# Kernel tuning notes

Measured on AMD Instinct MI355X. Metric: run time of the kernel, lower is better.

The kernel has to match this reference:

```python
import jax, jax.numpy as jnp
import numpy as np

EPS = 1e-6

def _rms(x, scale):
    # flax nn.RMSNorm: x / sqrt(mean(x^2)+eps) * scale, no mean subtraction
    return x * scale * jax.lax.rsqrt(jnp.mean(x * x, axis=-1, keepdims=True) + EPS)


def _forward(x, mem_k, mem_v, norm1_scale, norm2_scale,
             Wq, bq, Wk, bk, Wv, bv, Wz, bz,
             Wgz, bgz, Wgh, bgh,
             Wg1, bg1, Wg2, bg2, Wgc1, bgc1, Wgc2, bgc2,
             Awq, abq, Awk, abk, Awv, abv, Awo, abo,
             Wf1, bf1, Wf2, bf2):
    B, S, D = x.shape
    M = mem_k.shape[1]
    H = 8
    hd = D // H

    x_norm = _rms(x, norm1_scale)
    q = x_norm @ Wq + bq
    k = x_norm @ Wk + bk
    v = x_norm @ Wv + bv
    z = x_norm @ Wz + bz

    # input-dependent decay gamma in (1e-6, 1-1e-6)
    gamma_base = jax.nn.sigmoid(jax.nn.gelu(z @ Wg1 + bg1) @ Wg2 + bg2)
    gamma_mod = jax.nn.sigmoid(jax.nn.gelu(k @ Wgc1 + bgc1) @ Wgc2 + bgc2)
    gamma = jnp.clip(gamma_base * gamma_mod, 1e-6, 1.0 - 1e-6)

    # gated leaky recurrence over sequence: h depends on W_g_h(h_prev) -> strict scan
    def step(h_prev, zt_gt):
        z_t, g_t = zt_gt  # [B, D] each
        gate = jax.nn.sigmoid(z_t @ Wgz + bgz + h_prev @ Wgh + bgh)
        h_tilde = (1.0 - gate) * h_prev + gate * z_t
        h_t = h_tilde + g_t * h_prev
        return h_t, h_t

    h0 = jnp.zeros((B, D), dtype=x.dtype)
    z_T = jnp.swapaxes(z, 0, 1)          # [S, B, D]
    gamma_T = jnp.swapaxes(gamma, 0, 1)  # [S, B, D]
    _, h_seq_T = jax.lax.scan(step, h0, (z_T, gamma_T))
    h_seq = jnp.swapaxes(h_seq_T, 0, 1)  # [B, S, D]

    # MultiMemoryAttention: q from q_input, K/V from memory state banks [B, M, D]
    qh = (q @ Awq + abq).reshape(B, S, H, hd)
    kh = (mem_k @ Awk + abk).reshape(B, M, H, hd)
    vh = (mem_v @ Awv + abv).reshape(B, M, H, hd)
    scores = jnp.einsum('bshd,bmhd->bhsm', qh, kh) / jnp.sqrt(jnp.asarray(hd, x.dtype))
    probs = jax.nn.softmax(scores, axis=-1)
    mem_out = jnp.einsum('bhsm,bmhd->bshd', probs, vh).reshape(B, S, D) @ Awo + abo

    combined = h_seq + mem_out + v * 0.1
    x_res = x + combined  # dropout deterministic (training=False)

    x_norm2 = _rms(x_res, norm2_scale)
    ffn = jax.nn.gelu(x_norm2 @ Wf1 + bf1) @ Wf2 + bf2
    return x_res + ffn


def setup_inputs() -> dict:
    key = jax.random.key(0)
    B, S, D, H, F, M = 4, 4096, 1024, 8, 4096, 512
    Dq = D // 4
    ks = jax.random.split(key, 24)
    def w(i, shape):
        return jax.random.normal(ks[i], shape, dtype=jnp.float32) * 0.02
    d = {
        'x': jax.random.normal(ks[0], (B, S, D), dtype=jnp.float32),
        'mem_k': jax.random.normal(ks[1], (B, M, D), dtype=jnp.float32),
        'mem_v': jax.random.normal(ks[2], (B, M, D), dtype=jnp.float32),
        'norm1_scale': jnp.ones((D,), jnp.float32),
        'norm2_scale': jnp.ones((D,), jnp.float32),
        'Wq': w(3, (D, D)), 'bq': jnp.zeros((D,), jnp.float32),
        'Wk': w(4, (D, D)), 'bk': jnp.zeros((D,), jnp.float32),
        'Wv': w(5, (D, D)), 'bv': jnp.zeros((D,), jnp.float32),
        'Wz': w(6, (D, D)), 'bz': jnp.zeros((D,), jnp.float32),
        'Wgz': w(7, (D, D)), 'bgz': jnp.zeros((D,), jnp.float32),
        'Wgh': w(8, (D, D)), 'bgh': jnp.zeros((D,), jnp.float32),
        'Wg1': w(9, (D, Dq)), 'bg1': jnp.zeros((Dq,), jnp.float32),
        'Wg2': w(10, (Dq, D)), 'bg2': jnp.zeros((D,), jnp.float32),
        'Wgc1': w(11, (D, Dq)), 'bgc1': jnp.zeros((Dq,), jnp.float32),
        'Wgc2': w(12, (Dq, D)), 'bgc2': jnp.zeros((D,), jnp.float32),
        'Awq': w(13, (D, D)), 'abq': jnp.zeros((D,), jnp.float32),
        'Awk': w(14, (D, D)), 'abk': jnp.zeros((D,), jnp.float32),
        'Awv': w(15, (D, D)), 'abv': jnp.zeros((D,), jnp.float32),
        'Awo': w(16, (D, D)), 'abo': jnp.zeros((D,), jnp.float32),
        'Wf1': w(17, (D, F)), 'bf1': jnp.zeros((F,), jnp.float32),
        'Wf2': w(18, (F, D)), 'bf2': jnp.zeros((D,), jnp.float32),
    }
    return d


def reference(x, mem_k, mem_v, norm1_scale, norm2_scale,
              Wq, bq, Wk, bk, Wv, bv, Wz, bz,
              Wgz, bgz, Wgh, bgh,
              Wg1, bg1, Wg2, bg2, Wgc1, bgc1, Wgc2, bgc2,
              Awq, abq, Awk, abk, Awv, abv, Awo, abo,
              Wf1, bf1, Wf2, bf2):
    return _forward(x, mem_k, mem_v, norm1_scale, norm2_scale,
                    Wq, bq, Wk, bk, Wv, bv, Wz, bz,
                    Wgz, bgz, Wgh, bgh,
                    Wg1, bg1, Wg2, bg2, Wgc1, bgc1, Wgc2, bgc2,
                    Awq, abq, Awk, abk, Awv, abv, Awo, abo,
                    Wf1, bf1, Wf2, bf2)
```

## Files before the change

kernel.cpp:

```cpp
#include <hip/hip_runtime.h>
#include <stdint.h>

typedef short s16x8 __attribute__((ext_vector_type(8)));
typedef float f32x4 __attribute__((ext_vector_type(4)));

#define DEV static __device__ __forceinline__

DEV float bf2f(ushort u){ union{uint i;float f;}v; v.i=((uint)u)<<16; return v.f; }
DEV ushort f2bf(float f){ union{float f;uint i;}v; v.f=f; return (ushort)((v.i + 0x7FFFu + ((v.i>>16)&1u))>>16); }
DEV float fsigmoid(float x){ return 1.f/(1.f+__expf(-x)); }
DEV float fgelu(float x){
  float u = 0.7978845608028654f*(x + 0.044715f*x*x*x);
  float e = __expf(2.f*u);
  float th = 1.f - 2.f/(e+1.f);
  return 0.5f*x*(1.f+th);
}
DEV f32x4 mfma16(s16x8 a, s16x8 b, f32x4 c){
  return __builtin_amdgcn_mfma_f32_16x16x32_bf16(a,b,c,0,0,0);
}

__global__ __launch_bounds__(256) void transpose_cvt(const float* __restrict__ src,
                                                     ushort* __restrict__ dst, int K, int N){
  __shared__ float tile[64][65];
  int tk = blockIdx.y*64, tn = blockIdx.x*64;
  int t = threadIdx.x;
  int c4 = (t & 15)*4, r0 = t >> 4;
  #pragma unroll
  for (int p=0;p<4;++p){
    int r = r0 + p*16;
    float4 v = *(const float4*)(src + (size_t)(tk+r)*N + tn + c4);
    tile[r][c4+0]=v.x; tile[r][c4+1]=v.y; tile[r][c4+2]=v.z; tile[r][c4+3]=v.w;
  }
  __syncthreads();
  #pragma unroll
  for (int p=0;p<4;++p){
    int n = r0 + p*16;
    ushort4 o = make_ushort4(f2bf(tile[c4+0][n]), f2bf(tile[c4+1][n]),
                             f2bf(tile[c4+2][n]), f2bf(tile[c4+3][n]));
    *(ushort4*)(dst + (size_t)(tn+n)*K + tk + c4) = o;
  }
}

__global__ __launch_bounds__(256) void cvt_bf16(const float* __restrict__ s,
                                                ushort* __restrict__ d, int n){
  int i = (blockIdx.x*256 + threadIdx.x)*4;
  if (i < n){
    float4 v = *(const float4*)(s + i);
    ushort4 o = make_ushort4(f2bf(v.x), f2bf(v.y), f2bf(v.z), f2bf(v.w));
    *(ushort4*)(d + i) = o;
  }
}

__global__ __launch_bounds__(256) void bias_sum_k(const float* __restrict__ a,
                                                  const float* __restrict__ b,
                                                  float* __restrict__ o){
  int i = blockIdx.x*256 + threadIdx.x;
  if (i < 1024) o[i] = a[i] + b[i];
}

__global__ __launch_bounds__(256) void fuse_bias(const float* __restrict__ b_in,
                                                 const float* __restrict__ W,
                                                 const float* __restrict__ b_out,
                                                 float* __restrict__ o, int K, int N){
  int n = blockIdx.x*256 + threadIdx.x;
  if (n < N){
    float s = b_out[n];
    for (int k=0;k<K;++k) s += b_in[k]*W[(size_t)k*N + n];
    o[n] = s;
  }
}

__global__ __launch_bounds__(256) void rms_kernel(const float* __restrict__ x,
                                                  const float* __restrict__ scale,
                                                  ushort* __restrict__ out){
  int row = blockIdx.x, t = threadIdx.x;
  const float* xr = x + (size_t)row*1024;
  float4 v = *(const float4*)(xr + t*4);
  float ss = v.x*v.x + v.y*v.y + v.z*v.z + v.w*v.w;
  #pragma unroll
  for (int o=1;o<64;o<<=1) ss += __shfl_xor(ss, o);
  __shared__ float wsum[4];
  if ((t & 63)==0) wsum[t>>6] = ss;
  __syncthreads();
  float tot = wsum[0]+wsum[1]+wsum[2]+wsum[3];
  float rstd = rsqrtf(tot*(1.f/1024.f) + 1e-6f);
  float4 sc = *(const float4*)(scale + t*4);
  ushort4 o4 = make_ushort4(f2bf(v.x*sc.x*rstd), f2bf(v.y*sc.y*rstd),
                            f2bf(v.z*sc.z*rstd), f2bf(v.w*sc.w*rstd));
  *(ushort4*)(out + (size_t)row*1024 + t*4) = o4;
}

template<int EPI>
__global__ __launch_bounds__(256,2) void gemm_bf16(
    const ushort* __restrict__ A, const ushort* __restrict__ Bt,
    const float* __restrict__ bias, void* __restrict__ Cout,
    const void* __restrict__ aux0, const void* __restrict__ aux1,
    int M, int N, int K)
{
  __shared__ ushort Al[128*32];
  __shared__ ushort Bl[128*32];
  const int t = threadIdx.x, ln = t & 63;
  const int m0 = blockIdx.y*128, n0 = blockIdx.x*128;
  const int wv = t >> 6, wr = wv >> 1, wc = wv & 1;
  const int lr = ln & 15, lk = ln >> 4;
  f32x4 acc[4][4] = {};
  for (int kk = 0; kk < K; kk += 32) {
    #pragma unroll
    for (int cc = 0; cc < 2; ++cc) {
      int e = cc*256 + t;
      int r = e >> 2, sg = e & 3;
      s16x8 va = *(const s16x8*)(A  + (size_t)(m0+r)*K + kk + sg*8);
      s16x8 vb = *(const s16x8*)(Bt + (size_t)(n0+r)*K + kk + sg*8);
      *(s16x8*)&Al[e*8] = va;
      *(s16x8*)&Bl[e*8] = vb;
    }
    __syncthreads();
    s16x8 af[4], bfr[4];
    #pragma unroll
    for (int m=0;m<4;++m) af[m]  = *(const s16x8*)&Al[(wr*64 + m*16 + lr)*32 + lk*8];
    #pragma unroll
    for (int n=0;n<4;++n) bfr[n] = *(const s16x8*)&Bl[(wc*64 + n*16 + lr)*32 + lk*8];
    #pragma unroll
    for (int m=0;m<4;++m)
      #pragma unroll
      for (int n=0;n<4;++n)
        acc[m][n] = mfma16(af[m], bfr[n], acc[m][n]);
    __syncthreads();
  }
  #pragma unroll
  for (int m=0;m<4;++m){
    #pragma unroll
    for (int n=0;n<4;++n){
      #pragma unroll
      for (int j=0;j<4;++j){
        int row = m0 + wr*64 + m*16 + lk*4 + j;
        int col = n0 + wc*64 + n*16 + lr;
        float v = acc[m][n][j] + (bias ? bias[col] : 0.f);
        size_t idx = (size_t)row*N + col;
        if constexpr (EPI==0){ ((ushort*)Cout)[idx] = f2bf(v); }
        else if constexpr (EPI==1){ ((ushort*)Cout)[idx] = f2bf(fgelu(v)); }
        else if constexpr (EPI==2){ ((ushort*)Cout)[idx] = f2bf(fsigmoid(v)); }
        else if constexpr (EPI==3){
          float g = fsigmoid(v) * bf2f(((const ushort*)aux0)[idx]);
          g = fminf(fmaxf(g, 1e-6f), 1.f-1e-6f);
          ((ushort*)Cout)[idx] = f2bf(g);
        }
        else if constexpr (EPI==4){
          float o = v + ((const float*)aux0)[idx] + 0.1f*bf2f(((const ushort*)aux1)[idx]);
          ((float*)Cout)[idx] = o;
        }
        else if constexpr (EPI==5){ ((float*)Cout)[idx] += v; }
        else if constexpr (EPI==6){
          int bb = row >> 9, mm = row & 511, hh = col >> 7, dd = col & 127;
          ((ushort*)Cout)[ (((size_t)(bb*8 + hh)*128 + dd) << 9) + mm ] = f2bf(v);
        }
        else if constexpr (EPI==7){
          ((ushort*)Cout)[(size_t)col*M + row] = f2bf(v);
        }
      }
    }
  }
}

__global__ __launch_bounds__(256,1) void attn_kernel(
  const ushort* __restrict__ qh, const ushort* __restrict__ kh,
  const ushort* __restrict__ vhT, ushort* __restrict__ att)
{
  __shared__ ushort P[4*16*512];
  const int t = threadIdx.x, ln = t & 63, wv = t >> 6;
  const int lr = ln & 15, lk = ln >> 4;
  const int b = blockIdx.z, h = blockIdx.y, s0 = blockIdx.x*64;

  const ushort* qrow = qh + (size_t)(b*4096 + s0 + wv*16 + lr)*1024 + h*128 + lk*8;
  s16x8 qf[4];
  #pragma unroll
  for (int kt=0;kt<4;++kt) qf[kt] = *(const s16x8*)(qrow + kt*32);
  __syncthreads();

  f32x4 zero4 = {0.f,0.f,0.f,0.f};
  f32x4 sacc[32];
  #pragma unroll
  for (int i=0;i<32;++i) sacc[i] = zero4;

  const ushort* kbase = kh + (size_t)(b*512)*1024 + h*128 + lk*8;
  #pragma unroll
  for (int mt=0;mt<32;++mt){
    const ushort* krow = kbase + (size_t)(mt*16 + lr)*1024;
    #pragma unroll
    for (int kt=0;kt<4;++kt){
      s16x8 kf = *(const s16x8*)(krow + kt*32);
      sacc[mt] = mfma16(qf[kt], kf, sacc[mt]);
    }
  }
  const float scale = 0.08838834764831845f;
  float inv[4];
  #pragma unroll
  for (int j=0;j<4;++j){
    float m = -3.4e38f;
    #pragma unroll
    for (int mt=0;mt<32;++mt) m = fmaxf(m, sacc[mt][j]);
    m = fmaxf(m, __shfl_xor(m,1)); m = fmaxf(m, __shfl_xor(m,2));
    m = fmaxf(m, __shfl_xor(m,4)); m = fmaxf(m, __shfl_xor(m,8));
    float s = 0.f;
    #pragma unroll
    for (int mt=0;mt<32;++mt){
      float p = __expf((sacc[mt][j]-m)*scale);
      sacc[mt][j] = p; s += p;
    }
    s += __shfl_xor(s,1); s += __shfl_xor(s,2);
    s += __shfl_xor(s,4); s += __shfl_xor(s,8);
    inv[j] = 1.f/s;
  }
  char* pb = (char*)P + wv*16384;
  #pragma unroll
  for (int j=0;j<4;++j){
    int row = lk*4 + j;
    uint xr = (uint)((row & 7) << 4);
    #pragma unroll
    for (int mt=0;mt<32;++mt){
      int col = mt*16 + lr;
      *(ushort*)(pb + row*1024 + (((uint)(col*2)) ^ xr)) = f2bf(sacc[mt][j]);
    }
  }
  f32x4 oacc[8];
  #pragma unroll
  for (int i=0;i<8;++i) oacc[i] = zero4;
  const ushort* vb = vhT + (size_t)(b*8 + h)*128*512;
  const char* prow = (char*)P + wv*16384 + lr*1024;
  uint xrr = (uint)((lr & 7) << 4);
  #pragma unroll
  for (int km=0;km<16;++km){
    s16x8 pf = *(const s16x8*)(prow + (((uint)((km*32 + lk*8)*2)) ^ xrr));
    #pragma unroll
    for (int dt=0;dt<8;++dt){
      s16x8 vf = *(const s16x8*)(vb + (size_t)(dt*16 + lr)*512 + km*32 + lk*8);
      oacc[dt] = mfma16(pf, vf, oacc[dt]);
    }
  }
  ushort* ob = att + (size_t)(b*4096 + s0 + wv*16)*1024 + h*128;
  #pragma unroll
  for (int dt=0;dt<8;++dt){
    #pragma unroll
    for (int j=0;j<4;++j){
      int row = lk*4 + j, col = dt*16 + lr;
      ob[(size_t)row*1024 + col] = f2bf(oacc[dt][j]*inv[j]);
    }
  }
}

#define SCAN_NB 64
__global__ __launch_bounds__(256,1) void scan_kernel(
  const float* __restrict__ Wgh,
  const ushort* __restrict__ u_bf, const ushort* __restrict__ z_bf,
  const ushort* __restrict__ g_bf, float* __restrict__ xres,
  unsigned long long* __restrict__ h_buf)
{
  __shared__ ushort WL[16*1032];
  __shared__ ushort HL[5*1032];
  __shared__ float  red[4][16][4];
  const int t = threadIdx.x, blk = blockIdx.x;
  const int ln = t & 63, wv = t >> 6;

  {
    const int c = t & 15, i0 = (t >> 4) * 64;
    for (int j = 0; j < 64; ++j) {
      int i = i0 + j;
      WL[c*1032 + i] = f2bf(Wgh[(size_t)i*1024 + blk*16 + c]);
    }
  }
  for (int e = t; e < 1032; e += 256) HL[4*1032 + e] = 0;

  float hmine = 0.f;
  const int c_ep = t & 15, b_ep = t >> 4;
  float uu=0.f, zz=0.f, gg=0.f, xv=0.f;
  if (t < 64) {
    size_t i0 = ((size_t)(b_ep*4096))*1024 + blk*16 + c_ep;
    uu = bf2f(u_bf[i0]); zz = bf2f(z_bf[i0]); gg = bf2f(g_bf[i0]); xv = xres[i0];
  }
  __syncthreads();

  const int arow = ln & 15, akc = ln >> 4;
  const ushort* Abase = &HL[(arow < 4 ? arow : 4)*1032 + akc*8];
  const ushort* Bbase = &WL[(ln & 15)*1032 + akc*8];
  const int hb_t = t >> 6, hk0 = (t & 63)*16;

  for (int step = 0; step < 4096; ++step) {
    {
      const unsigned long long* hs = h_buf + (size_t)(step & 1)*2048 + t*8;
      unsigned long long v[8];
      #pragma unroll
      for (int j = 0; j < 8; ++j)
        v[j] = __hip_atomic_load(hs + j, __ATOMIC_RELAXED, __HIP_MEMORY_SCOPE_AGENT);
      while (true) {
        uint bad = 0;
        #pragma unroll
        for (int j = 0; j < 8; ++j)
          if ((uint)(v[j] >> 32) != (uint)step) bad |= (1u << j);
        if (!bad) break;
        #pragma unroll
        for (int j = 0; j < 8; ++j)
          if (bad & (1u << j))
            v[j] = __hip_atomic_load(hs + j, __ATOMIC_RELAXED, __HIP_MEMORY_SCOPE_AGENT);
      }
      uint* dst = (uint*)&HL[hb_t*1032 + hk0];
      *(uint4*)(dst + 0) = make_uint4((uint)v[0], (uint)v[1], (uint)v[2], (uint)v[3]);
      *(uint4*)(dst + 4) = make_uint4((uint)v[4], (uint)v[5], (uint)v[6], (uint)v[7]);
    }
    __syncthreads();
    f32x4 acc = {0.f,0.f,0.f,0.f};
    #pragma unroll
    for (int m = 0; m < 8; ++m) {
      int koff = wv*256 + m*32;
      s16x8 a = *(const s16x8*)(Abase + koff);
      s16x8 b = *(const s16x8*)(Bbase + koff);
      acc = mfma16(a, b, acc);
    }
    if (ln < 16) *(f32x4*)&red[wv][ln][0] = acc;
    __syncthreads();
    if (t < 64) {
      float y = red[0][c_ep][b_ep] + red[1][c_ep][b_ep]
              + red[2][c_ep][b_ep] + red[3][c_ep][b_ep];
      float gate = fsigmoid(y + uu);
      float hn = hmine + gate*(zz - hmine) + gg*hmine;
      hmine = hn;
      int colg = blk*16 + c_ep;
      float hup = __shfl_down(hn, 1);
      if ((t & 1) == 0) {
        unsigned long long pk = ((unsigned long long)(uint)(step+1) << 32)
                              | ((uint)f2bf(hup) << 16) | (uint)f2bf(hn);
        __hip_atomic_store(h_buf + (size_t)((step+1)&1)*2048 + b_ep*512 + (colg>>1), pk,
                           __ATOMIC_RELAXED, __HIP_MEMORY_SCOPE_AGENT);
      }
      size_t idx = ((size_t)(b_ep*4096 + step))*1024 + colg;
      xres[idx] = xv + hn;
      int sn = (step+1 < 4096) ? step+1 : 4095;
      size_t idxn = ((size_t)(b_ep*4096 + sn))*1024 + colg;
      uu = bf2f(u_bf[idxn]); zz = bf2f(z_bf[idxn]); gg = bf2f(g_bf[idxn]);
      xv = xres[idxn];
    }
  }
}

extern "C" void kernel_launch(void* const* d_in, const int* in_sizes, int n_in,
                              void* d_out, int out_size, void* d_ws, size_t ws_size,
                              hipStream_t stream)
{
  const float* x    = (const float*)d_in[0];
  const float* memk = (const float*)d_in[1];
  const float* memv = (const float*)d_in[2];
  const float* n1s  = (const float*)d_in[3];
  const float* n2s  = (const float*)d_in[4];
  const float* Wq = (const float*)d_in[5];   const float* bq = (const float*)d_in[6];
  const float* Wk = (const float*)d_in[7];   const float* bk = (const float*)d_in[8];
  const float* Wv = (const float*)d_in[9];   const float* bv = (const float*)d_in[10];
  const float* Wz = (const float*)d_in[11];  const float* bz = (const float*)d_in[12];
  const float* Wgz = (const float*)d_in[13]; const float* bgz = (const float*)d_in[14];
  const float* Wgh = (const float*)d_in[15]; const float* bgh = (const float*)d_in[16];
  const float* Wg1 = (const float*)d_in[17]; const float* bg1 = (const float*)d_in[18];
  const float* Wg2 = (const float*)d_in[19]; const float* bg2 = (const float*)d_in[20];
  const float* Wgc1 = (const float*)d_in[21]; const float* bgc1 = (const float*)d_in[22];
  const float* Wgc2 = (const float*)d_in[23]; const float* bgc2 = (const float*)d_in[24];
  const float* Awq = (const float*)d_in[25]; const float* abq = (const float*)d_in[26];
  const float* Awk = (const float*)d_in[27]; const float* abk = (const float*)d_in[28];
  const float* Awv = (const float*)d_in[29]; const float* abv = (const float*)d_in[30];
  const float* Awo = (const float*)d_in[31]; const float* abo = (const float*)d_in[32];
  const float* Wf1 = (const float*)d_in[33]; const float* bf1 = (const float*)d_in[34];
  const float* Wf2 = (const float*)d_in[35]; const float* bf2 = (const float*)d_in[36];
  (void)in_sizes; (void)n_in; (void)out_size; (void)ws_size;

  char* ws = (char*)d_ws;
  constexpr size_t MB = 1ull<<20;
  ushort* WvT     = (ushort*)(ws + 0*MB);
  ushort* WzT     = (ushort*)(ws + 2*MB);
  ushort* WgzT    = (ushort*)(ws + 4*MB);
  ushort* WqAwqT  = (ushort*)(ws + 6*MB);
  ushort* AwkT    = (ushort*)(ws + 8*MB);
  ushort* AwvT    = (ushort*)(ws + 10*MB);
  ushort* AwoT    = (ushort*)(ws + 12*MB);
  ushort* Wf1T    = (ushort*)(ws + 14*MB);
  ushort* Wf2Tc   = (ushort*)(ws + 22*MB);
  ushort* Wg1T    = (ushort*)(ws + 30*MB);
  ushort* Wg2T    = (ushort*)(ws + 30*MB + 512*1024);
  ushort* Wgc2T   = (ushort*)(ws + 31*MB);
  ushort* WkWgc1T = (ushort*)(ws + 31*MB + 512*1024);
  float* bsum = (float*)(ws + 32*MB);
  float* bqh  = (float*)(ws + 32*MB + 4096);
  float* bkg  = (float*)(ws + 32*MB + 8192);
  char*  scanB = ws + 32*MB + 65536;
  ushort* Abuf = (ushort*)(ws + 33*MB);
  ushort* Bbuf = (ushort*)(ws + 65*MB);
  ushort* Cbuf = (ushort*)(ws + 97*MB);
  ushort* Dbuf = (ushort*)(ws + 129*MB);
  ushort* Ebuf = (ushort*)(ws + 161*MB);
  char* db = (char*)d_out;
  ushort* t1B   = (ushort*)(db + 0);
  ushort* memkB = (ushort*)(db + 8*MB);
  ushort* memvB = (ushort*)(db + 12*MB);
  ushort* khB   = (ushort*)(db + 16*MB);
  ushort* vhTB  = (ushort*)(db + 20*MB);
  ushort* gbB   = (ushort*)(db + 24*MB);
  ushort* WtmpB = (ushort*)(db + 56*MB);
  ushort* BtTB  = (ushort*)(db + 58*MB);

  const int M1 = 16384;
  dim3 b256(256);
  auto T = [&](const float* s, ushort* d, int K, int N){
    transpose_cvt<<<dim3(N/64, K/64), b256, 0, stream>>>(s, d, K, N);
  };
  #define G(EPI, Ap, Bp, bi, Cp, a0, a1, Mv, Nv, Kv) \
    gemm_bf16<EPI><<<dim3((Nv)/128,(Mv)/128), b256, 0, stream>>>( \
      (const ushort*)(Ap), (const ushort*)(Bp), bi, (void*)(Cp), a0, a1, Mv, Nv, Kv)

  cvt_bf16<<<1024, b256, 0, stream>>>(Wq, WtmpB, 1048576);
  T(Awq, BtTB, 1024, 1024);
  G(7, WtmpB, BtTB, nullptr, WqAwqT, nullptr, nullptr, 1024, 1024, 1024);
  fuse_bias<<<4, b256, 0, stream>>>(bq, Awq, abq, bqh, 1024, 1024);
  cvt_bf16<<<1024, b256, 0, stream>>>(Wk, WtmpB, 1048576);
  T(Wgc1, BtTB, 1024, 256);
  G(7, WtmpB, BtTB, nullptr, WkWgc1T, nullptr, nullptr, 1024, 256, 1024);
  fuse_bias<<<1, b256, 0, stream>>>(bk, Wgc1, bgc1, bkg, 1024, 256);
  T(Wv,WvT,1024,1024); T(Wz,WzT,1024,1024); T(Wgz,WgzT,1024,1024);
  T(Wg1,Wg1T,1024,256); T(Wg2,Wg2T,256,1024); T(Wgc2,Wgc2T,256,1024);
  T(Awk,AwkT,1024,1024); T(Awv,AwvT,1024,1024); T(Awo,AwoT,1024,1024);
  T(Wf1,Wf1T,1024,4096);
  for (int cch = 0; cch < 4; ++cch)
    T(Wf2 + (size_t)cch*1048576, Wf2Tc + (size_t)cch*1048576, 1024, 1024);
  bias_sum_k<<<4, b256, 0, stream>>>(bgz, bgh, bsum);
  cvt_bf16<<<2048, b256, 0, stream>>>(memk, memkB, 2097152);
  cvt_bf16<<<2048, b256, 0, stream>>>(memv, memvB, 2097152);

  rms_kernel<<<M1, b256, 0, stream>>>(x, n1s, Abuf);
  G(0, Abuf, WzT, bz, Bbuf, nullptr, nullptr, M1, 1024, 1024);
  G(0, Abuf, WvT, bv, Cbuf, nullptr, nullptr, M1, 1024, 1024);
  G(0, Abuf, WqAwqT, bqh, Dbuf, nullptr, nullptr, M1, 1024, 1024);
  G(0, Bbuf, WgzT, bsum, Ebuf, nullptr, nullptr, M1, 1024, 1024);
  G(1, Bbuf, Wg1T, bg1, t1B, nullptr, nullptr, M1, 256, 1024);
  G(2, t1B, Wg2T, bg2, gbB, nullptr, nullptr, M1, 1024, 256);
  G(1, Abuf, WkWgc1T, bkg, t1B, nullptr, nullptr, M1, 256, 1024);
  G(3, t1B, Wgc2T, bgc2, Abuf, gbB, nullptr, M1, 1024, 256);
  G(0, memkB, AwkT, abk, khB, nullptr, nullptr, 2048, 1024, 1024);
  G(6, memvB, AwvT, abv, vhTB, nullptr, nullptr, 2048, 1024, 1024);
  attn_kernel<<<dim3(64,8,4), b256, 0, stream>>>(Dbuf, khB, vhTB, Dbuf);
  G(4, Dbuf, AwoT, abo, d_out, (const void*)x, (const void*)Cbuf, M1, 1024, 1024);
  hipMemsetAsync(scanB, 0, 32768, stream);
  scan_kernel<<<SCAN_NB, b256, 0, stream>>>(Wgh, Ebuf, Bbuf, Abuf, (float*)d_out,
                                            (unsigned long long*)scanB);
  rms_kernel<<<M1, b256, 0, stream>>>((const float*)d_out, n2s, Cbuf);
  for (int cch = 0; cch < 4; ++cch) {
    G(1, Cbuf, Wf1T + (size_t)cch*1048576, bf1 + cch*1024, Dbuf, nullptr, nullptr, M1, 1024, 1024);
    G(5, Dbuf, Wf2Tc + (size_t)cch*1048576, (cch==0 ? bf2 : nullptr), d_out, nullptr, nullptr, M1, 1024, 1024);
  }
  #undef G
}
```

Baseline: 13.31 ms.

## Process scan batches separately to pipeline cross-block h exchange per batch

The scan kernel now splits each time step into four per-batch sub-steps. Each sub-step waits only on that batch's slice of the shared h buffer and prefetches the next batch's slice while the current matmul runs. This is meant to let blocks run on partial data instead of waiting for all four batches, hiding the cross-block flag latency. In exchange there are four times as many __syncthreads and MFMA passes per step, with only one useful row per pass.

```diff
diff --git a/kernel.cpp b/kernel.cpp
--- a/kernel.cpp
+++ b/kernel.cpp
@@ -256,87 +256,90 @@
   unsigned long long* __restrict__ h_buf)
 {
   __shared__ ushort WL[16*1032];
-  __shared__ ushort HL[5*1032];
-  __shared__ float  red[4][16][4];
+  __shared__ ushort HL[2*1032];
+  __shared__ float  red[4][16];
   const int t = threadIdx.x, blk = blockIdx.x;
   const int ln = t & 63, wv = t >> 6;
 
   {
-    const int c = t & 15, i0 = (t >> 4) * 64;
+    const int c = t & 15, i0q = (t >> 4) * 64;
     for (int j = 0; j < 64; ++j) {
-      int i = i0 + j;
+      int i = i0q + j;
       WL[c*1032 + i] = f2bf(Wgh[(size_t)i*1024 + blk*16 + c]);
     }
   }
-  for (int e = t; e < 1032; e += 256) HL[4*1032 + e] = 0;
-
-  float hmine = 0.f;
-  const int c_ep = t & 15, b_ep = t >> 4;
-  float uu=0.f, zz=0.f, gg=0.f, xv=0.f;
-  if (t < 64) {
-    size_t i0 = ((size_t)(b_ep*4096))*1024 + blk*16 + c_ep;
-    uu = bf2f(u_bf[i0]); zz = bf2f(z_bf[i0]); gg = bf2f(g_bf[i0]); xv = xres[i0];
-  }
+  for (int e = t; e < 1032; e += 256) HL[1032 + e] = 0;
+
+  float hst[4] = {0.f,0.f,0.f,0.f};
+  float uu[4], zz[4], gg[4], xv[4];
+  if (t < 16) {
+    #pragma unroll
+    for (int b=0;b<4;++b){
+      size_t i0 = ((size_t)(b*4096))*1024 + blk*16 + t;
+      uu[b]=bf2f(u_bf[i0]); zz[b]=bf2f(z_bf[i0]);
+      gg[b]=bf2f(g_bf[i0]); xv[b]=xres[i0];
+    }
+  }
+  const int arow = ln & 15, akc = ln >> 4;
+  const ushort* Ab = (arow == 0) ? &HL[akc*8] : &HL[1032 + akc*8];
+  const ushort* Bb = &WL[arow*1032 + akc*8];
+
+  unsigned long long p0, p1;
+  p0 = __hip_atomic_load(h_buf + t*2 + 0, __ATOMIC_RELAXED, __HIP_MEMORY_SCOPE_AGENT);
+  p1 = __hip_atomic_load(h_buf + t*2 + 1, __ATOMIC_RELAXED, __HIP_MEMORY_SCOPE_AGENT);
   __syncthreads();
 
-  const int arow = ln & 15, akc = ln >> 4;
-  const ushort* Abase = &HL[(arow < 4 ? arow : 4)*1032 + akc*8];
-  const ushort* Bbase = &WL[(ln & 15)*1032 + akc*8];
-  const int hb_t = t >> 6, hk0 = (t & 63)*16;
-
-  for (int step = 0; step < 4096; ++step) {
-    {
-      const unsigned long long* hs = h_buf + (size_t)(step & 1)*2048 + t*8;
-      unsigned long long v[8];
+  for (int s = 0; s < 4096; ++s) {
+    #pragma unroll
+    for (int b = 0; b < 4; ++b) {
+      const unsigned long long* hs =
+        h_buf + (size_t)((s & 1)*2048 + b*512) + t*2;
+      while (((uint)(p0 >> 32) != (uint)s) | ((uint)(p1 >> 32) != (uint)s)) {
+        if ((uint)(p0 >> 32) != (uint)s)
+          p0 = __hip_atomic_load(hs + 0, __ATOMIC_RELAXED, __HIP_MEMORY_SCOPE_AGENT);
+        if ((uint)(p1 >> 32) != (uint)s)
+          p1 = __hip_atomic_load(hs + 1, __ATOMIC_RELAXED, __HIP_MEMORY_SCOPE_AGENT);
+      }
+      *(uint2*)&HL[t*4] = make_uint2((uint)p0, (uint)p1);
+      {
+        const int nb = (b + 1) & 3;
+        const int ns = s + (b == 3 ? 1 : 0);
+        const unsigned long long* hn =
+          h_buf + (size_t)((ns & 1)*2048 + nb*512) + t*2;
+        p0 = __hip_atomic_load(hn + 0, __ATOMIC_RELAXED, __HIP_MEMORY_SCOPE_AGENT);
+        p1 = __hip_atomic_load(hn + 1, __ATOMIC_RELAXED, __HIP_MEMORY_SCOPE_AGENT);
+      }
+      __syncthreads();
+      f32x4 acc = {0.f,0.f,0.f,0.f};
       #pragma unroll
-      for (int j = 0; j < 8; ++j)
-        v[j] = __hip_atomic_load(hs + j, __ATOMIC_RELAXED, __HIP_MEMORY_SCOPE_AGENT);
-      while (true) {
-        uint bad = 0;
-        #pragma unroll
-        for (int j = 0; j < 8; ++j)
-          if ((uint)(v[j] >> 32) != (uint)step) bad |= (1u << j);
-        if (!bad) break;
-        #pragma unroll
-        for (int j = 0; j < 8; ++j)
-          if (bad & (1u << j))
-            v[j] = __hip_atomic_load(hs + j, __ATOMIC_RELAXED, __HIP_MEMORY_SCOPE_AGENT);
+      for (int m = 0; m < 8; ++m) {
+        int koff = wv*256 + m*32;
+        s16x8 a  = *(const s16x8*)(Ab + koff);
+        s16x8 w8 = *(const s16x8*)(Bb + koff);
+        acc = mfma16(a, w8, acc);
       }
-      uint* dst = (uint*)&HL[hb_t*1032 + hk0];
-      *(uint4*)(dst + 0) = make_uint4((uint)v[0], (uint)v[1], (uint)v[2], (uint)v[3]);
-      *(uint4*)(dst + 4) = make_uint4((uint)v[4], (uint)v[5], (uint)v[6], (uint)v[7]);
-    }
-    __syncthreads();
-    f32x4 acc = {0.f,0.f,0.f,0.f};
-    #pragma unroll
-    for (int m = 0; m < 8; ++m) {
-      int koff = wv*256 + m*32;
-      s16x8 a = *(const s16x8*)(Abase + koff);
-      s16x8 b = *(const s16x8*)(Bbase + koff);
-      acc = mfma16(a, b, acc);
-    }
-    if (ln < 16) *(f32x4*)&red[wv][ln][0] = acc;
-    __syncthreads();
-    if (t < 64) {
-      float y = red[0][c_ep][b_ep] + red[1][c_ep][b_ep]
-              + red[2][c_ep][b_ep] + red[3][c_ep][b_ep];
-      float gate = fsigmoid(y + uu);
-      float hn = hmine + gate*(zz - hmine) + gg*hmine;
-      hmine = hn;
-      int colg = blk*16 + c_ep;
-      float hup = __shfl_down(hn, 1);
-      if ((t & 1) == 0) {
-        unsigned long long pk = ((unsigned long long)(uint)(step+1) << 32)
-                              | ((uint)f2bf(hup) << 16) | (uint)f2bf(hn);
-        __hip_atomic_store(h_buf + (size_t)((step+1)&1)*2048 + b_ep*512 + (colg>>1), pk,
-                           __ATOMIC_RELAXED, __HIP_MEMORY_SCOPE_AGENT);
+      if (ln < 16) red[wv][ln] = acc[0];
+      __syncthreads();
+      if (t < 16) {
+        float y = red[0][t] + red[1][t] + red[2][t] + red[3][t];
+        float gate = fsigmoid(y + uu[b]);
+        float hnv = hst[b] + gate*(zz[b] - hst[b]) + gg[b]*hst[b];
+        hst[b] = hnv;
+        int colg = blk*16 + t;
+        float hup = __shfl_down(hnv, 1);
+        if ((t & 1) == 0) {
+          unsigned long long pk = ((unsigned long long)(uint)(s + 1) << 32)
+                                | ((uint)f2bf(hup) << 16) | (uint)f2bf(hnv);
+          __hip_atomic_store(h_buf + (size_t)(((s + 1) & 1)*2048 + b*512) + (colg >> 1),
+                             pk, __ATOMIC_RELAXED, __HIP_MEMORY_SCOPE_AGENT);
+        }
+        size_t idx = ((size_t)(b*4096 + s))*1024 + colg;
+        xres[idx] = xv[b] + hnv;
+        int sn = (s + 1 < 4096) ? s + 1 : 4095;
+        size_t idxn = ((size_t)(b*4096 + sn))*1024 + colg;
+        uu[b]=bf2f(u_bf[idxn]); zz[b]=bf2f(z_bf[idxn]);
+        gg[b]=bf2f(g_bf[idxn]); xv[b]=xres[idxn];
       }
-      size_t idx = ((size_t)(b_ep*4096 + step))*1024 + colg;
-      xres[idx] = xv + hn;
-      int sn = (step+1 < 4096) ? step+1 : 4095;
-      size_t idxn = ((size_t)(b_ep*4096 + sn))*1024 + colg;
-      uu = bf2f(u_bf[idxn]); zz = bf2f(z_bf[idxn]); gg = bf2f(g_bf[idxn]);
-      xv = xres[idxn];
     }
   }
 }
```

Measured after the change: 16.76 ms. 1.26x slower.

## Pin recurrent scan to 16 workgroups on a single XCD

Applied to the files above, without the earlier changes.

The sequential scan now launches 256 workgroups. Each reads its XCC ID, and only the first 16 that land on the same XCD as block 0 become workers; the rest exit. Each worker owns 64 output columns instead of 16, so each wave does the full 1024-wide K reduction itself rather than reducing across waves through shared memory. Keeping all exchange of h on one XCD is meant to make the per-step cross-workgroup handoff go through a shared L2 instead of across dies, at the cost of fewer CUs doing the per-step matvec and an extra barrier per step. The scheme also depends on 16 workgroups landing on that XCD and running at the same time; otherwise the spin waits never finish.

```diff
diff --git a/kernel.cpp b/kernel.cpp
--- a/kernel.cpp
+++ b/kernel.cpp
@@ -17,6 +17,11 @@
 }
 DEV f32x4 mfma16(s16x8 a, s16x8 b, f32x4 c){
   return __builtin_amdgcn_mfma_f32_16x16x32_bf16(a,b,c,0,0,0);
+}
+DEV uint get_xcc_id(){
+  uint v;
+  asm volatile("s_getreg_b32 %0, hwreg(HW_REG_XCC_ID)" : "=s"(v));
+  return v;
 }
 
 __global__ __launch_bounds__(256) void transpose_cvt(const float* __restrict__ src,
@@ -248,41 +253,64 @@
   }
 }
 
-#define SCAN_NB 64
+#define SCAN_WORKERS 16
 __global__ __launch_bounds__(256,1) void scan_kernel(
   const float* __restrict__ Wgh,
   const ushort* __restrict__ u_bf, const ushort* __restrict__ z_bf,
   const ushort* __restrict__ g_bf, float* __restrict__ xres,
-  unsigned long long* __restrict__ h_buf)
+  unsigned long long* __restrict__ h_buf, uint* __restrict__ claim)
 {
-  __shared__ ushort WL[16*1032];
+  __shared__ ushort WL[64*1032];
   __shared__ ushort HL[5*1032];
-  __shared__ float  red[4][16][4];
-  const int t = threadIdx.x, blk = blockIdx.x;
+  __shared__ int s_wid;
+  const int t = threadIdx.x;
+
+  if (t == 0) {
+    uint xcd = get_xcc_id();
+    if (blockIdx.x == 0)
+      __hip_atomic_store(claim, xcd + 1u, __ATOMIC_RELAXED, __HIP_MEMORY_SCOPE_AGENT);
+    uint tgt;
+    do { tgt = __hip_atomic_load(claim, __ATOMIC_RELAXED, __HIP_MEMORY_SCOPE_AGENT); }
+    while (tgt == 0u);
+    int wid = -1;
+    if (xcd == tgt - 1u) {
+      uint tk = __hip_atomic_fetch_add(claim + 1, 1u, __ATOMIC_RELAXED,
+                                       __HIP_MEMORY_SCOPE_AGENT);
+      if (tk < SCAN_WORKERS) wid = (int)tk;
+    }
+    s_wid = wid;
+  }
+  __syncthreads();
+  const int wid = s_wid;
+  if (wid < 0) return;
+
   const int ln = t & 63, wv = t >> 6;
-
   {
-    const int c = t & 15, i0 = (t >> 4) * 64;
-    for (int j = 0; j < 64; ++j) {
-      int i = i0 + j;
-      WL[c*1032 + i] = f2bf(Wgh[(size_t)i*1024 + blk*16 + c]);
+    const int c = t & 63, i0q = (t >> 6) * 256;
+    for (int j = 0; j < 256; ++j) {
+      int i = i0q + j;
+      WL[c*1032 + i] = f2bf(Wgh[(size_t)i*1024 + wid*64 + c]);
     }
   }
   for (int e = t; e < 1032; e += 256) HL[4*1032 + e] = 0;
 
-  float hmine = 0.f;
-  const int c_ep = t & 15, b_ep = t >> 4;
-  float uu=0.f, zz=0.f, gg=0.f, xv=0.f;
-  if (t < 64) {
-    size_t i0 = ((size_t)(b_ep*4096))*1024 + blk*16 + c_ep;
-    uu = bf2f(u_bf[i0]); zz = bf2f(z_bf[i0]); gg = bf2f(g_bf[i0]); xv = xres[i0];
+  const int lr = ln & 15, lk = ln >> 4;
+  const ushort* Abase = &HL[(lr < 4 ? lr : 4)*1032 + lk*8];
+  const ushort* Bbase = &WL[(wv*16 + lr)*1032 + lk*8];
+  const int hb_t = t >> 6, hk0 = (t & 63)*16;
+  const int colg = wid*64 + wv*16 + lr;
+
+  float hst[4] = {0.f,0.f,0.f,0.f};
+  float uu[4], zz[4], gg[4], xv[4];
+  if (ln < 16) {
+    #pragma unroll
+    for (int j=0;j<4;++j){
+      size_t i0 = ((size_t)(j*4096))*1024 + colg;
+      uu[j]=bf2f(u_bf[i0]); zz[j]=bf2f(z_bf[i0]);
+      gg[j]=bf2f(g_bf[i0]); xv[j]=xres[i0];
+    }
   }
   __syncthreads();
-
-  const int arow = ln & 15, akc = ln >> 4;
-  const ushort* Abase = &HL[(arow < 4 ? arow : 4)*1032 + akc*8];
-  const ushort* Bbase = &WL[(ln & 15)*1032 + akc*8];
-  const int hb_t = t >> 6, hk0 = (t & 63)*16;
 
   for (int step = 0; step < 4096; ++step) {
     {
@@ -302,41 +330,44 @@
           if (bad & (1u << j))
             v[j] = __hip_atomic_load(hs + j, __ATOMIC_RELAXED, __HIP_MEMORY_SCOPE_AGENT);
       }
+      __syncthreads();
       uint* dst = (uint*)&HL[hb_t*1032 + hk0];
       *(uint4*)(dst + 0) = make_uint4((uint)v[0], (uint)v[1], (uint)v[2], (uint)v[3]);
       *(uint4*)(dst + 4) = make_uint4((uint)v[4], (uint)v[5], (uint)v[6], (uint)v[7]);
     }
     __syncthreads();
-    f32x4 acc = {0.f,0.f,0.f,0.f};
-    #pragma unroll
-    for (int m = 0; m < 8; ++m) {
-      int koff = wv*256 + m*32;
-      s16x8 a = *(const s16x8*)(Abase + koff);
-      s16x8 b = *(const s16x8*)(Bbase + koff);
-      acc = mfma16(a, b, acc);
-    }
-    if (ln < 16) *(f32x4*)&red[wv][ln][0] = acc;
-    __syncthreads();
-    if (t < 64) {
-      float y = red[0][c_ep][b_ep] + red[1][c_ep][b_ep]
-              + red[2][c_ep][b_ep] + red[3][c_ep][b_ep];
-      float gate = fsigmoid(y + uu);
-      float hn = hmine + gate*(zz - hmine) + gg*hmine;
-      hmine = hn;
-      int colg = blk*16 + c_ep;
-      float hup = __shfl_down(hn, 1);
-      if ((t & 1) == 0) {
-        unsigned long long pk = ((unsigned long long)(uint)(step+1) << 32)
-                              | ((uint)f2bf(hup) << 16) | (uint)f2bf(hn);
-        __hip_atomic_store(h_buf + (size_t)((step+1)&1)*2048 + b_ep*512 + (colg>>1), pk,
-                           __ATOMIC_RELAXED, __HIP_MEMORY_SCOPE_AGENT);
+    f32x4 a0 = {0.f,0.f,0.f,0.f}, a1 = a0, a2 = a0, a3 = a0;
+    #pragma unroll
+    for (int m = 0; m < 32; m += 4) {
+      a0 = mfma16(*(const s16x8*)(Abase + (m+0)*32), *(const s16x8*)(Bbase + (m+0)*32), a0);
+      a1 = mfma16(*(const s16x8*)(Abase + (m+1)*32), *(const s16x8*)(Bbase + (m+1)*32), a1);
+      a2 = mfma16(*(const s16x8*)(Abase + (m+2)*32), *(const s16x8*)(Bbase + (m+2)*32), a2);
+      a3 = mfma16(*(const s16x8*)(Abase + (m+3)*32), *(const s16x8*)(Bbase + (m+3)*32), a3);
+    }
+    f32x4 acc = (a0 + a1) + (a2 + a3);
+    if (ln < 16) {
+      #pragma unroll
+      for (int j=0;j<4;++j){
+        float gate = fsigmoid(acc[j] + uu[j]);
+        float hn = hst[j] + gate*(zz[j] - hst[j]) + gg[j]*hst[j];
+        hst[j] = hn;
+        float hup = __shfl_down(hn, 1);
+        if ((ln & 1) == 0) {
+          unsigned long long pk = ((unsigned long long)(uint)(step+1) << 32)
+                                | ((uint)f2bf(hup) << 16) | (uint)f2bf(hn);
+          __hip_atomic_store(h_buf + (size_t)(((step+1)&1)*2048 + j*512) + (colg>>1),
+                             pk, __ATOMIC_RELAXED, __HIP_MEMORY_SCOPE_AGENT);
+        }
+        size_t idx = ((size_t)(j*4096 + step))*1024 + colg;
+        xres[idx] = xv[j] + hn;
       }
-      size_t idx = ((size_t)(b_ep*4096 + step))*1024 + colg;
-      xres[idx] = xv + hn;
       int sn = (step+1 < 4096) ? step+1 : 4095;
-      size_t idxn = ((size_t)(b_ep*4096 + sn))*1024 + colg;
-      uu = bf2f(u_bf[idxn]); zz = bf2f(z_bf[idxn]); gg = bf2f(g_bf[idxn]);
-      xv = xres[idxn];
+      #pragma unroll
+      for (int j=0;j<4;++j){
+        size_t idxn = ((size_t)(j*4096 + sn))*1024 + colg;
+        uu[j]=bf2f(u_bf[idxn]); zz[j]=bf2f(z_bf[idxn]);
+        gg[j]=bf2f(g_bf[idxn]); xv[j]=xres[idxn];
+      }
     }
   }
 }
@@ -442,9 +473,9 @@
   G(6, memvB, AwvT, abv, vhTB, nullptr, nullptr, 2048, 1024, 1024);
   attn_kernel<<<dim3(64,8,4), b256, 0, stream>>>(Dbuf, khB, vhTB, Dbuf);
   G(4, Dbuf, AwoT, abo, d_out, (const void*)x, (const void*)Cbuf, M1, 1024, 1024);
-  hipMemsetAsync(scanB, 0, 32768, stream);
-  scan_kernel<<<SCAN_NB, b256, 0, stream>>>(Wgh, Ebuf, Bbuf, Abuf, (float*)d_out,
-                                            (unsigned long long*)scanB);
+  hipMemsetAsync(scanB, 0, 33024, stream);
+  scan_kernel<<<256, b256, 0, stream>>>(Wgh, Ebuf, Bbuf, Abuf, (float*)d_out,
+                                        (unsigned long long*)scanB, (uint*)(scanB + 32768));
   rms_kernel<<<M1, b256, 0, stream>>>((const float*)d_out, n2s, Cbuf);
   for (int cch = 0; cch < 4; ++cch) {
     G(1, Cbuf, Wf1T + (size_t)cch*1048576, bf1 + cch*1024, Dbuf, nullptr, nullptr, M1, 1024, 1024);
```

After: 14.08 ms. 1.06x slower.
